# Optimization experiments

Measured on AMD Instinct MI355X. Metric: run time of the kernel, lower is better.

Reference implementation:

```python
import jax, jax.numpy as jnp
import numpy as np
from jax import lax
from jax.scipy.stats import norm

K = 2            # top-k
NUM_EXPERTS = 4
NOISE_EPS = 0.01
LOSS_COEF = 0.01


def conv3x3(x, w):
    # x: [B,Cin,H,W], w: [Cout,Cin,3,3] -> [B,Cout,H,W]
    return lax.conv_general_dilated(x, w, (1, 1), 'SAME',
                                    dimension_numbers=('NCHW', 'OIHW', 'NCHW'))


def setup_inputs() -> dict:
    key = jax.random.key(0)
    ks = jax.random.split(key, 16)
    B, C, H, W = 16, 3, 256, 256
    FC = 2 * C                      # freq channels = 6
    HID = 64
    D = H * W * C                   # flattened gating dim = 196608
    f32 = jnp.float32
    inp = {
        'x':   jax.random.normal(ks[0], (B, C, H, W), f32),
        'ref': jax.random.normal(ks[1], (B, C, H, W), f32),
        'noise': jax.random.normal(ks[2], (B, NUM_EXPERTS), f32),
        'mod_w1': (jax.random.normal(ks[3], (FC, 2 * FC), f32) * 0.1),
        'mod_b1': jnp.zeros((FC,), f32),
        'mod_w2': (jax.random.normal(ks[4], (FC, FC), f32) * 0.1),
        'mod_b2': jnp.zeros((FC,), f32),
        'enh_w': (jax.random.normal(ks[5], (FC, FC), f32) * 0.1),
        'enh_b': jnp.zeros((FC,), f32),
        'fre_prompt': (jax.random.normal(ks[6], (FC, H, W // 2 + 1), f32) * 0.1),
        'w_gate':  (jax.random.normal(ks[7], (D, NUM_EXPERTS), f32) * 0.002),
        'w_noise': (jax.random.normal(ks[8], (D, NUM_EXPERTS), f32) * 0.002),
        'ew1': (jax.random.normal(ks[9],  (NUM_EXPERTS, HID, C, 3, 3), f32) * 0.05),
        'eb1': jnp.zeros((NUM_EXPERTS, HID), f32),
        'ew2': (jax.random.normal(ks[10], (NUM_EXPERTS, 1, HID, 3, 3), f32) * 0.05),
        'eb2': jnp.zeros((NUM_EXPERTS, 1), f32),
    }
    return inp


def _cv_squared(v):
    # torch .var() is unbiased (ddof=1)
    return jnp.var(v, ddof=1) / (jnp.mean(v) ** 2 + 1e-10)


def _forward(x, ref, noise, mod_w1, mod_b1, mod_w2, mod_b2, enh_w, enh_b,
             fre_prompt, w_gate, w_noise, ew1, eb1, ew2, eb2):
    B, C, H, W = x.shape

    # ---- frequency_prompt(ref) ----
    fft = jnp.fft.rfft2(ref, norm='ortho')                    # [B,C,H,W//2+1]
    freq = jnp.concatenate([fft.real, fft.imag], axis=1)      # [B,2C,H,Wf]
    # Adaptive avg/max pool to (H, W//2+1) are identities at native size
    pooled = jnp.concatenate([freq, freq], axis=1)            # [B,4C,H,Wf]
    m = jnp.einsum('oi,bihw->bohw', mod_w1, pooled) + mod_b1[:, None, None]
    m = jax.nn.relu(m)
    m = jnp.einsum('oi,bihw->bohw', mod_w2, m) + mod_b2[:, None, None]
    enh = m * fre_prompt[None]                                # [B,2C,H,Wf]
    enh = jax.nn.relu(jnp.einsum('oi,bihw->bohw', enh_w, enh) + enh_b[:, None, None])
    re, im = jnp.split(enh, 2, axis=1)
    spatial = jnp.fft.irfft2(re + 1j * im, s=(H, W), norm='ortho')  # [B,C,H,W]
    prompt = jax.nn.softmax(spatial.mean(axis=(2, 3), keepdims=True), axis=1)  # [B,C,1,1]

    # ---- noisy top-k gating ----
    x_ds = (x * prompt + x).reshape(B, -1)                    # [B, H*W*C]
    clean_logits = x_ds @ w_gate                              # [B,E]
    noise_stddev = jax.nn.softplus(x_ds @ w_noise) + NOISE_EPS
    noisy_logits = clean_logits + noise * noise_stddev
    top_vals, top_idx = lax.top_k(noisy_logits, K + 1)        # sorted desc, [B,K+1]
    tk_gates = jax.nn.softmax(top_vals[:, :K], axis=1)        # [B,K]
    gates = jnp.zeros_like(noisy_logits).at[
        jnp.arange(B)[:, None], top_idx[:, :K]].set(tk_gates)  # [B,E]

    # load = prob each expert's noisy logit lands in top-k
    thr_in = top_vals[:, K:K + 1]
    thr_out = top_vals[:, K - 1:K]
    is_in = noisy_logits > thr_in
    prob = jnp.where(is_in,
                     norm.cdf((clean_logits - thr_in) / noise_stddev),
                     norm.cdf((clean_logits - thr_out) / noise_stddev))
    load = prob.sum(0)
    importance = gates.sum(0)
    loss = (_cv_squared(importance) + _cv_squared(load)) * LOSS_COEF

    # ---- expert dispatch/combine (== weighted sum; gates are 0 off top-k) ----
    y = jnp.zeros((B, ew2.shape[1], H, W), x.dtype)
    for e in range(NUM_EXPERTS):
        h = jax.nn.relu(conv3x3(x, ew1[e]) + eb1[e][None, :, None, None])
        o = conv3x3(h, ew2[e]) + eb2[e][None, :, None, None]
        y = y + gates[:, e][:, None, None, None] * o
    return y, loss


def reference(x, ref, noise, mod_w1, mod_b1, mod_w2, mod_b2, enh_w, enh_b,
              fre_prompt, w_gate, w_noise, ew1, eb1, ew2, eb2):
    return _forward(x, ref, noise, mod_w1, mod_b1, mod_w2, mod_b2, enh_w, enh_b,
                    fre_prompt, w_gate, w_noise, ew1, eb1, ew2, eb2)
```

## Files before the change

kernel.cpp:

```cpp
#include <hip/hip_runtime.h>
#include <hip/hip_bf16.h>
#include <math.h>

#define WS_GATE 192
#define WS_GNP  256
#define WS_W1F  25088
#define WS_W2F  29184
#define WS_B1P  31616

typedef float    float4v __attribute__((ext_vector_type(4)));
typedef short    short8v __attribute__((ext_vector_type(8)));
typedef _Float16 half8v  __attribute__((ext_vector_type(8)));
typedef _Float16 half2v  __attribute__((ext_vector_type(2)));

union Q4 { uint4 q; short8v s; half8v h; };
union H2 { unsigned u; half2v h; };

__device__ __forceinline__ unsigned short bf16b(float f) {
    unsigned u = __builtin_bit_cast(unsigned, f);
    u = (u + 0x7FFFu + ((u >> 16) & 1u)) >> 16;
    return (unsigned short)u;
}

__device__ __forceinline__ unsigned pkbf16(float a, float b) {
#if __has_builtin(__builtin_amdgcn_cvt_pk_bf16_f32)
    return __builtin_bit_cast(unsigned, __builtin_amdgcn_cvt_pk_bf16_f32(a, b));
#else
    return (unsigned)bf16b(a) | ((unsigned)bf16b(b) << 16);
#endif
}

__device__ __forceinline__ unsigned pkf16(float a, float b) {
#if __has_builtin(__builtin_amdgcn_cvt_pkrtz)
    return __builtin_bit_cast(unsigned, __builtin_amdgcn_cvt_pkrtz(a, b));
#else
    union { _Float16 h[2]; unsigned u; } p;
    p.h[0] = (_Float16)a; p.h[1] = (_Float16)b;
    return p.u;
#endif
}

__device__ __forceinline__ half2v pkmax0(half2v a) {
#if __has_builtin(__builtin_elementwise_max)
    return __builtin_elementwise_max(a, (half2v){(_Float16)0, (_Float16)0});
#else
    half2v r;
    r[0] = a[0] > (_Float16)0 ? a[0] : (_Float16)0;
    r[1] = a[1] > (_Float16)0 ? a[1] : (_Float16)0;
    return r;
#endif
}

__device__ __forceinline__ void wave_fence() {
    asm volatile("s_waitcnt lgkmcnt(0)" ::: "memory");
}

__global__ void k_aux(const float* __restrict__ ref, const float* __restrict__ x,
                      const float* __restrict__ wg,  const float* __restrict__ wn,
                      const float* __restrict__ ew1, const float* __restrict__ ew2,
                      const float* __restrict__ eb1,
                      float* __restrict__ ws) {
    __shared__ float sh[4][16][8];
    int blk = blockIdx.x, t = threadIdx.x;

    if (blk < 192) {
        int bc = blk >> 2, chunk = blk & 3;
        const float4* p4 = (const float4*)(ref + (size_t)bc*65536 + (size_t)chunk*16384);
        float acc = 0.f;
        #pragma unroll
        for (int i = 0; i < 16; ++i) { float4 v = p4[i*256 + t]; acc += v.x + v.y + v.z + v.w; }
        #pragma unroll
        for (int m = 1; m <= 32; m <<= 1) acc += __shfl_xor(acc, m);
        if ((t & 63) == 0) sh[0][0][t >> 6] = acc;
        __syncthreads();
        if (t == 0) ws[bc*4 + chunk] = sh[0][0][0] + sh[0][0][1] + sh[0][0][2] + sh[0][0][3];
        return;
    }
    if (blk < 384) {
        int r = blk - 192;
        int c = r >> 6, chunk = r & 63;
        int lane = t & 63, wv = t >> 6;
        int hw0 = chunk*1024 + t*4;
        const float4* wg4 = (const float4*)wg;
        const float4* wn4 = (const float4*)wn;
        const float4* x4  = (const float4*)x;
        float4 G[4], Nw[4];
        #pragma unroll
        for (int i = 0; i < 4; ++i) {
            G[i]  = wg4[c*65536 + hw0 + i];
            Nw[i] = wn4[c*65536 + hw0 + i];
        }
        for (int b = 0; b < 16; ++b) {
            float4 xv = x4[(b*3 + c)*16384 + chunk*256 + t];
            float xs[4] = {xv.x, xv.y, xv.z, xv.w};
            float aG[4] = {0,0,0,0}, aN[4] = {0,0,0,0};
            #pragma unroll
            for (int i = 0; i < 4; ++i) {
                aG[0] += xs[i]*G[i].x;  aG[1] += xs[i]*G[i].y;
                aG[2] += xs[i]*G[i].z;  aG[3] += xs[i]*G[i].w;
                aN[0] += xs[i]*Nw[i].x; aN[1] += xs[i]*Nw[i].y;
                aN[2] += xs[i]*Nw[i].z; aN[3] += xs[i]*Nw[i].w;
            }
            #pragma unroll
            for (int m = 1; m <= 32; m <<= 1) {
                #pragma unroll
                for (int e = 0; e < 4; ++e) {
                    aG[e] += __shfl_xor(aG[e], m);
                    aN[e] += __shfl_xor(aN[e], m);
                }
            }
            if (lane == 0) {
                #pragma unroll
                for (int e = 0; e < 4; ++e) { sh[wv][b][e] = aG[e]; sh[wv][b][4+e] = aN[e]; }
            }
        }
        __syncthreads();
        if (t < 128) {
            int b = t >> 3, s = t & 7;
            float v = sh[0][b][s] + sh[1][b][s] + sh[2][b][s] + sh[3][b][s];
            atomicAdd(&ws[WS_GNP + (b*3 + c)*8 + s], v);
        }
        return;
    }
    uint4* w1f = (uint4*)(ws + WS_W1F);
    for (int i = t; i < 1024; i += 256) {
        int mm = i & 15, r = i >> 4, qq = r & 3, r2 = r >> 2, f = r2 & 3, e = r2 >> 2;
        const float* w1 = ew1 + e*1728 + (f*16 + mm)*27 + qq*8;
        int navail = 27 - qq*8;
        float v[8];
        #pragma unroll
        for (int j = 0; j < 8; ++j) v[j] = (j < navail) ? w1[j] : 0.f;
        uint4 q;
        q.x = pkbf16(v[0], v[1]); q.y = pkbf16(v[2], v[3]);
        q.z = pkbf16(v[4], v[5]); q.w = pkbf16(v[6], v[7]);
        w1f[i] = q;
    }
    uint4* w2f = (uint4*)(ws + WS_W2F);
    for (int i = t; i < 512; i += 256) {
        int qq = i & 3, r = i >> 2, ks = r & 1, r2 = r >> 1, mm = r2 & 15, e = r2 >> 4;
        uint4 q = make_uint4(0, 0, 0, 0);
        if (mm < 9) {
            float v[8];
            #pragma unroll
            for (int j = 0; j < 8; ++j) v[j] = ew2[e*576 + (ks*32 + qq*8 + j)*9 + mm];
            q.x = pkf16(v[0], v[1]); q.y = pkf16(v[2], v[3]);
            q.z = pkf16(v[4], v[5]); q.w = pkf16(v[6], v[7]);
        }
        w2f[i] = q;
    }
    uint2* b1p = (uint2*)(ws + WS_B1P);
    if (t < 64) {
        int qq = t & 3, r = t >> 2, f = r & 3, e = r >> 2;
        const float* bb = eb1 + e*64 + f*16 + qq*4;
        b1p[t] = make_uint2(pkf16(bb[0], bb[1]), pkf16(bb[2], bb[3]));
    }
}

__global__ void k_gating(const float* __restrict__ noise,
                         const float* __restrict__ mw1, const float* __restrict__ mb1,
                         const float* __restrict__ mw2, const float* __restrict__ mb2,
                         const float* __restrict__ enw, const float* __restrict__ enb,
                         const float* __restrict__ fp,
                         float* __restrict__ ws, float* __restrict__ out) {
    __shared__ float GN2[48*8];
    __shared__ float gL[16][4], pL[16][4], cvs[2];
    int t = threadIdx.x;
    #pragma unroll
    for (int u = 0; u < 3; ++u) {
        int idx = t*3 + u;
        GN2[idx] = ws[WS_GNP + idx];
    }
    __syncthreads();
    if (t < 16) {
        int b = t;
        float sc[3];
        for (int c = 0; c < 3; ++c) {
            int bc = b*3 + c;
            sc[c] = (ws[bc*4] + ws[bc*4+1] + ws[bc*4+2] + ws[bc*4+3]) * (1.f/256.f);
        }
        float pooled[12];
        for (int i = 0; i < 12; ++i) { int r = i % 6; pooled[i] = (r < 3) ? sc[r] : 0.f; }
        float m1[6];
        for (int o = 0; o < 6; ++o) {
            float a = mb1[o];
            for (int i = 0; i < 12; ++i) a += mw1[o*12 + i] * pooled[i];
            m1[o] = fmaxf(a, 0.f);
        }
        float m2[6];
        for (int o = 0; o < 6; ++o) {
            float a = mb2[o];
            for (int i = 0; i < 6; ++i) a += mw2[o*6 + i] * m1[i];
            m2[o] = a * fp[(size_t)o * 33024];
        }
        float dc[3];
        for (int o = 0; o < 3; ++o) {
            float a = enb[o];
            for (int i = 0; i < 6; ++i) a += enw[o*6 + i] * m2[i];
            dc[o] = fmaxf(a, 0.f) * (1.f/256.f);
        }
        float mx = fmaxf(dc[0], fmaxf(dc[1], dc[2]));
        float e0 = expf(dc[0]-mx), e1 = expf(dc[1]-mx), e2 = expf(dc[2]-mx);
        float inv = 1.f / (e0 + e1 + e2);
        float pc[3] = { e0*inv + 1.f, e1*inv + 1.f, e2*inv + 1.f };
        float cl[4], sg[4], nz[4];
        for (int e = 0; e < 4; ++e) {
            float a = 0.f, nr = 0.f;
            for (int c = 0; c < 3; ++c) {
                a  += pc[c] * GN2[(b*3 + c)*8 + e];
                nr += pc[c] * GN2[(b*3 + c)*8 + 4 + e];
            }
            cl[e] = a;
            float sp = (nr > 20.f) ? nr : log1pf(expf(nr));
            sg[e] = sp + 0.01f;
            nz[e] = a + noise[b*4 + e] * sg[e];
        }
        int i0 = 0; float v0 = nz[0];
        for (int e = 1; e < 4; ++e) if (nz[e] > v0) { v0 = nz[e]; i0 = e; }
        int i1 = -1; float v1 = -3.4e38f;
        for (int e = 0; e < 4; ++e) if (e != i0 && nz[e] > v1) { v1 = nz[e]; i1 = e; }
        float v2 = -3.4e38f;
        for (int e = 0; e < 4; ++e) if (e != i0 && e != i1 && nz[e] > v2) v2 = nz[e];
        float ex = expf(v1 - v0), den = 1.f + ex;
        float gate[4] = {0.f, 0.f, 0.f, 0.f};
        gate[i0] = 1.f/den; gate[i1] = ex/den;
        for (int e = 0; e < 4; ++e) {
            ws[WS_GATE + b*4 + e] = gate[e];
            gL[b][e] = gate[e];
            float thr = (nz[e] > v2) ? v2 : v1;
            pL[b][e] = 0.5f * (1.f + erff((cl[e] - thr) / sg[e] * 0.70710678118f));
        }
    }
    __syncthreads();
    if (t < 2) {
        float v[4];
        for (int e = 0; e < 4; ++e) {
            float s = 0.f;
            for (int b = 0; b < 16; ++b) s += (t == 0) ? gL[b][e] : pL[b][e];
            v[e] = s;
        }
        float mean = 0.25f * (v[0] + v[1] + v[2] + v[3]);
        float var = 0.f;
        for (int e = 0; e < 4; ++e) { float d = v[e] - mean; var += d*d; }
        var *= (1.f/3.f);
        cvs[t] = var / (mean*mean + 1e-10f);
    }
    __syncthreads();
    if (t == 0) out[1048576] = (cvs[0] + cvs[1]) * 0.01f;
}

__global__ __launch_bounds__(256, 4)
void k_experts(const float* __restrict__ x, const float* __restrict__ eb2,
               const float* __restrict__ ws, float* __restrict__ out) {
    __shared__ __align__(16) float in_s[1200];
    __shared__ __align__(16) uint4 s_exch[4][16][9];
    __shared__ __align__(16) float s_T[4][9][116];

    int t = threadIdx.x;
    int bid = blockIdx.x;
    int logical = (bid & 7) * 512 + (bid >> 3);
    int b = logical >> 8, tile = logical & 255;
    int ty0 = (tile >> 4) * 16, tx0 = (tile & 15) * 16;
    const float* xb = x + (size_t)b * 196608;

    for (int i = t; i < 1200; i += 256) {
        int ci = i / 400, r = i - ci*400, iy = r / 20, ix = r - iy*20;
        int gy = ty0 - 2 + iy, gx = tx0 - 2 + ix;
        float v = 0.f;
        if ((unsigned)gy < 256u && (unsigned)gx < 256u) v = xb[ci*65536 + gy*256 + gx];
        in_s[i] = v;
    }
    __syncthreads();

    int lane = t & 63, wv = t >> 6;
    int qq = lane >> 4, mm = lane & 15;

    int offj[8];
    #pragma unroll
    for (int j = 0; j < 8; ++j) {
        int k = qq*8 + j;
        if (k < 27) { int ci = k/9, r = k - ci*9, kh = r/3, kw = r - kh*3;
                      offj[j] = ci*400 + kh*20 + kw; }
        else offj[j] = -1;
    }

    bool interior = (ty0 > 0) && (ty0 < 240) && (tx0 > 0) && (tx0 < 240);

    Q4 bfr[7];
    H2 mskg[7];
    #pragma unroll
    for (int grp = 0; grp < 7; ++grp) {
        int p = wv*72 + grp*16 + mm;
        int py = p/18, px = p - py*18;
        int base = (p < 324) ? (py*20 + px) : 0;
        float v[8];
        #pragma unroll
        for (int j = 0; j < 8; ++j)
            v[j] = (offj[j] >= 0) ? in_s[base + offj[j]] : 0.f;
        bfr[grp].q.x = pkbf16(v[0], v[1]); bfr[grp].q.y = pkbf16(v[2], v[3]);
        bfr[grp].q.z = pkbf16(v[4], v[5]); bfr[grp].q.w = pkbf16(v[6], v[7]);
        if (!interior) {
            int gy = ty0 - 1 + py, gx = tx0 - 1 + px;
            float msk = (((unsigned)gy < 256u) && ((unsigned)gx < 256u)) ? 1.f : 0.f;
            mskg[grp].u = pkf16(msk, msk);
        }
    }

    const float4 gates = *(const float4*)(ws + WS_GATE + b*4);
    float gv[4] = {gates.x, gates.y, gates.z, gates.w};
    const uint4* w1f = (const uint4*)(ws + WS_W1F);
    const uint4* w2f = (const uint4*)(ws + WS_W2F);
    const uint2* b1p = (const uint2*)(ws + WS_B1P);

    uint2* exw = (uint2*)&s_exch[wv][mm][0];
    const uint4* exr = &s_exch[wv][mm][0];
    float accY = 0.f;

    for (int e = 0; e < 4; ++e) {
        float gval = gv[e];
        if (gval == 0.f) continue;

        Q4 bw0, bw1;
        bw0.q = w2f[((e*16 + mm)*2 + 0)*4 + qq];
        bw1.q = w2f[((e*16 + mm)*2 + 1)*4 + qq];
        Q4 af[4]; H2 b01[4], b23[4];
        #pragma unroll
        for (int f = 0; f < 4; ++f) {
            af[f].q = w1f[((e*4 + f)*4 + qq)*16 + mm];
            uint2 bp = b1p[(e*4 + f)*4 + qq];
            b01[f].u = bp.x; b23[f].u = bp.y;
        }

        #pragma unroll
        for (int grp = 0; grp < 7; ++grp) {
            #pragma unroll
            for (int f = 0; f < 4; ++f) {
                float4v d = __builtin_amdgcn_mfma_f32_16x16x32_bf16(
                    af[f].s, bfr[grp].s, (float4v){0.f,0.f,0.f,0.f}, 0, 0, 0);
                H2 h01, h23;
                h01.u = pkf16(d[0], d[1]);
                h23.u = pkf16(d[2], d[3]);
                h01.h = pkmax0(h01.h + b01[f].h);
                h23.h = pkmax0(h23.h + b23[f].h);
                if (!interior) { h01.h = h01.h * mskg[grp].h; h23.h = h23.h * mskg[grp].h; }
                exw[f*4 + qq] = make_uint2(h01.u, h23.u);
            }
            wave_fence();

            Q4 a0, a1;
            a0.q = exr[qq];
            a1.q = exr[4 + qq];
            float4v d2 = __builtin_amdgcn_mfma_f32_16x16x32_f16(
                a0.h, bw0.h, (float4v){0.f,0.f,0.f,0.f}, 0, 0, 0);
            d2 = __builtin_amdgcn_mfma_f32_16x16x32_f16(a1.h, bw1.h, d2, 0, 0, 0);
            if (mm < 9)
                *(float4*)&s_T[wv][mm][grp*16 + qq*4] = make_float4(d2[0], d2[1], d2[2], d2[3]);
            wave_fence();
        }

        float oacc = 0.f;
        #pragma unroll
        for (int kh = 0; kh < 3; ++kh) {
            #pragma unroll
            for (int kw = 0; kw < 3; ++kw)
                oacc += s_T[wv][kh*3 + kw][(qq + kh)*18 + mm + kw];
        }
        wave_fence();
        accY += gval * (oacc + eb2[e]);
    }
    out[(size_t)b*65536 + (ty0 + wv*4 + qq)*256 + tx0 + mm] = accY;
}

extern "C" void kernel_launch(void* const* d_in, const int* in_sizes, int n_in,
                              void* d_out, int out_size, void* d_ws, size_t ws_size,
                              hipStream_t stream) {
    (void)in_sizes; (void)n_in; (void)out_size; (void)ws_size;
    const float* x     = (const float*)d_in[0];
    const float* ref   = (const float*)d_in[1];
    const float* noise = (const float*)d_in[2];
    const float* mw1   = (const float*)d_in[3];
    const float* mb1   = (const float*)d_in[4];
    const float* mw2   = (const float*)d_in[5];
    const float* mb2   = (const float*)d_in[6];
    const float* enw   = (const float*)d_in[7];
    const float* enb   = (const float*)d_in[8];
    const float* fp    = (const float*)d_in[9];
    const float* wg    = (const float*)d_in[10];
    const float* wn    = (const float*)d_in[11];
    const float* ew1   = (const float*)d_in[12];
    const float* eb1   = (const float*)d_in[13];
    const float* ew2   = (const float*)d_in[14];
    const float* eb2   = (const float*)d_in[15];
    float* out = (float*)d_out;
    float* ws  = (float*)d_ws;

    hipMemsetAsync(ws + WS_GNP, 0, 384*sizeof(float), stream);
    k_aux    <<<385, 256, 0, stream>>>(ref, x, wg, wn, ew1, ew2, eb1, ws);
    k_gating <<<1, 128, 0, stream>>>(noise, mw1, mb1, mw2, mb2, enw, enb, fp, ws, out);
    k_experts<<<4096, 256, 0, stream>>>(x, eb2, ws, out);
}
```

Measured before the change: 172.8 us.

## Keep expert hidden activations in registers via permuted weights; alias LDS for occupancy

The first-layer expert weights and biases are repacked with a channel permutation. This makes the first MFMA's output fragment match the operand layout of the second MFMA, so hidden activations go straight into registers instead of through a per-wave LDS exchange with fences. The input tile and the output staging buffer now share one LDS allocation, separated by a barrier, and launch bounds are raised to allow more resident blocks. Separately, the gating partial sums are written per chunk and reduced in the gating kernel, which removes the memset and the atomics. The costs are more register pressure and a serial 64-way reduction in a single-block kernel.

Measured after the change: 177.7 us. +2.9%, slower.

```diff
diff --git a/kernel.cpp b/kernel.cpp
--- a/kernel.cpp
+++ b/kernel.cpp
@@ -118,14 +118,15 @@
         if (t < 128) {
             int b = t >> 3, s = t & 7;
             float v = sh[0][b][s] + sh[1][b][s] + sh[2][b][s] + sh[3][b][s];
-            atomicAdd(&ws[WS_GNP + (b*3 + c)*8 + s], v);
+            ws[WS_GNP + ((size_t)(c*64 + chunk)*16 + b)*8 + s] = v;
         }
         return;
     }
     uint4* w1f = (uint4*)(ws + WS_W1F);
     for (int i = t; i < 1024; i += 256) {
         int mm = i & 15, r = i >> 4, qq = r & 3, r2 = r >> 2, f = r2 & 3, e = r2 >> 2;
-        const float* w1 = ew1 + e*1728 + (f*16 + mm)*27 + qq*8;
+        int chan = (mm >> 2)*8 + (f & 1)*4 + (mm & 3) + (f >> 1)*32;
+        const float* w1 = ew1 + e*1728 + chan*27 + qq*8;
         int navail = 27 - qq*8;
         float v[8];
         #pragma unroll
@@ -151,7 +152,7 @@
     uint2* b1p = (uint2*)(ws + WS_B1P);
     if (t < 64) {
         int qq = t & 3, r = t >> 2, f = r & 3, e = r >> 2;
-        const float* bb = eb1 + e*64 + f*16 + qq*4;
+        const float* bb = eb1 + e*64 + qq*8 + (f & 1)*4 + (f >> 1)*32;
         b1p[t] = make_uint2(pkf16(bb[0], bb[1]), pkf16(bb[2], bb[3]));
     }
 }
@@ -168,7 +169,13 @@
     #pragma unroll
     for (int u = 0; u < 3; ++u) {
         int idx = t*3 + u;
-        GN2[idx] = ws[WS_GNP + idx];
+        int bc = idx >> 3, s = idx & 7;
+        int b = bc / 3, c = bc - b*3;
+        float v = 0.f;
+        #pragma unroll 8
+        for (int ch = 0; ch < 64; ++ch)
+            v += ws[WS_GNP + ((size_t)(c*64 + ch)*16 + b)*8 + s];
+        GN2[bc*8 + s] = v;
     }
     __syncthreads();
     if (t < 16) {
@@ -248,12 +255,13 @@
     if (t == 0) out[1048576] = (cvs[0] + cvs[1]) * 0.01f;
 }
 
-__global__ __launch_bounds__(256, 4)
+__global__ __launch_bounds__(256, 6)
 void k_experts(const float* __restrict__ x, const float* __restrict__ eb2,
                const float* __restrict__ ws, float* __restrict__ out) {
-    __shared__ __align__(16) float in_s[1200];
-    __shared__ __align__(16) uint4 s_exch[4][16][9];
-    __shared__ __align__(16) float s_T[4][9][116];
+    __shared__ __align__(16) char s_raw[16704];
+    float* in_s = (float*)s_raw;
+    typedef float sT_t[9][116];
+    sT_t* s_T = (sT_t*)s_raw;
 
     int t = threadIdx.x;
     int bid = blockIdx.x;
@@ -304,15 +312,13 @@
             mskg[grp].u = pkf16(msk, msk);
         }
     }
+    __syncthreads();
 
     const float4 gates = *(const float4*)(ws + WS_GATE + b*4);
     float gv[4] = {gates.x, gates.y, gates.z, gates.w};
     const uint4* w1f = (const uint4*)(ws + WS_W1F);
     const uint4* w2f = (const uint4*)(ws + WS_W2F);
     const uint2* b1p = (const uint2*)(ws + WS_B1P);
-
-    uint2* exw = (uint2*)&s_exch[wv][mm][0];
-    const uint4* exr = &s_exch[wv][mm][0];
     float accY = 0.f;
 
     for (int e = 0; e < 4; ++e) {
@@ -332,6 +338,7 @@
 
         #pragma unroll
         for (int grp = 0; grp < 7; ++grp) {
+            Q4 a0, a1;
             #pragma unroll
             for (int f = 0; f < 4; ++f) {
                 float4v d = __builtin_amdgcn_mfma_f32_16x16x32_bf16(
@@ -342,20 +349,18 @@
                 h01.h = pkmax0(h01.h + b01[f].h);
                 h23.h = pkmax0(h23.h + b23[f].h);
                 if (!interior) { h01.h = h01.h * mskg[grp].h; h23.h = h23.h * mskg[grp].h; }
-                exw[f*4 + qq] = make_uint2(h01.u, h23.u);
+                if      (f == 0) { a0.q.x = h01.u; a0.q.y = h23.u; }
+                else if (f == 1) { a0.q.z = h01.u; a0.q.w = h23.u; }
+                else if (f == 2) { a1.q.x = h01.u; a1.q.y = h23.u; }
+                else             { a1.q.z = h01.u; a1.q.w = h23.u; }
             }
-            wave_fence();
-
-            Q4 a0, a1;
-            a0.q = exr[qq];
-            a1.q = exr[4 + qq];
             float4v d2 = __builtin_amdgcn_mfma_f32_16x16x32_f16(
                 a0.h, bw0.h, (float4v){0.f,0.f,0.f,0.f}, 0, 0, 0);
             d2 = __builtin_amdgcn_mfma_f32_16x16x32_f16(a1.h, bw1.h, d2, 0, 0, 0);
             if (mm < 9)
                 *(float4*)&s_T[wv][mm][grp*16 + qq*4] = make_float4(d2[0], d2[1], d2[2], d2[3]);
-            wave_fence();
-        }
+        }
+        wave_fence();
 
         float oacc = 0.f;
         #pragma unroll
@@ -393,7 +398,6 @@
     float* out = (float*)d_out;
     float* ws  = (float*)d_ws;
 
-    hipMemsetAsync(ws + WS_GNP, 0, 384*sizeof(float), stream);
     k_aux    <<<385, 256, 0, stream>>>(ref, x, wg, wn, ew1, ew2, eb1, ws);
     k_gating <<<1, 128, 0, stream>>>(noise, mw1, mb1, mw2, mb2, enw, enb, fp, ws, out);
     k_experts<<<4096, 256, 0, stream>>>(x, eb2, ws, out);
```
